# Kernel tuning notes

Measured on AMD Instinct MI355X. Metric: run time of the kernel, lower is better.

The kernel has to match this reference:

```python
import jax, jax.numpy as jnp
import numpy as np

N_NODES = 50000
N_EDGES = 600000
N_SUB = 20000
E_SUB = 120000
D = 128

def setup_inputs() -> dict:
    key = jax.random.key(0)
    ks = jax.random.split(key, 16)
    s = 1.0 / np.sqrt(D)
    inp = {
        "x": jax.random.normal(ks[0], (N_NODES, D), dtype=jnp.float32),
        "Wm": jax.random.normal(ks[1], (D, D), dtype=jnp.float32) * s,
        "bm": jnp.zeros((D,), dtype=jnp.float32),
        "Wn2s0": jax.random.normal(ks[2], (D, D), dtype=jnp.float32) * s,
        "bn2s0": jnp.zeros((D,), dtype=jnp.float32),
        "Ws2n0": jax.random.normal(ks[3], (D, D), dtype=jnp.float32) * s,
        "bs2n0": jnp.zeros((D,), dtype=jnp.float32),
        "Wn2s1": jax.random.normal(ks[4], (D, D), dtype=jnp.float32) * s,
        "bn2s1": jnp.zeros((D,), dtype=jnp.float32),
        "Ws2n1": jax.random.normal(ks[5], (D, D), dtype=jnp.float32) * s,
        "bs2n1": jnp.zeros((D,), dtype=jnp.float32),
        "neighbor_edge_index": jax.random.randint(ks[6], (2, N_EDGES), 0, N_NODES, dtype=jnp.int64),
        "sub_row0": jax.random.randint(ks[7], (E_SUB,), 0, N_NODES, dtype=jnp.int64),
        "sub_col0": jax.random.randint(ks[8], (E_SUB,), 0, N_SUB, dtype=jnp.int64),
        "sub_row1": jax.random.randint(ks[9], (E_SUB,), 0, N_NODES, dtype=jnp.int64),
        "sub_col1": jax.random.randint(ks[10], (E_SUB,), 0, N_SUB, dtype=jnp.int64),
    }
    return inp


def _level(x, row, col, Wn2s, bn2s, Ws2n, bs2n):
    # node -> substructure: gather node feats, sum-reduce into substructures
    sub_x = jax.ops.segment_sum(x[row], col, num_segments=N_SUB)  # [n_sub, D]
    sub_x = sub_x @ Wn2s + bn2s
    # substructure -> node: gather substructure feats, sum-reduce back to nodes
    msg = jax.ops.segment_sum(sub_x[col], row, num_segments=N_NODES)  # [N, D]
    msg = msg @ Ws2n + bs2n
    return x + msg


def reference(x, Wm, bm, Wn2s0, bn2s0, Ws2n0, bs2n0, Wn2s1, bn2s1, Ws2n1, bs2n1,
              neighbor_edge_index, sub_row0, sub_col0, sub_row1, sub_col1):
    src, dst = neighbor_edge_index[0], neighbor_edge_index[1]
    # message_neighbor: GIN-like sum aggregation + Linear + ReLU
    agg = jax.ops.segment_sum(x[src], dst, num_segments=N_NODES)
    x = jax.nn.relu((x + agg) @ Wm + bm)
    # substructure levels (gather -> scatter-sum -> Linear -> gather -> scatter-sum -> Linear -> residual)
    x = _level(x, sub_row0, sub_col0, Wn2s0, bn2s0, Ws2n0, bs2n0)
    x = _level(x, sub_row1, sub_col1, Wn2s1, bn2s1, Ws2n1, bs2n1)
    return x
```

## Files before the change

kernel.cpp:

```cpp
#include <hip/hip_runtime.h>

#define D 128
#define NN 50000
#define NS 20000
#define NNP 50048
#define NSP 20032
#define L_TOT (3 * NN + 2 * NS)
#define LDA 136

#define NB_BKT 188
#define CBUF_SLOTS 1296384
#define HIST_CHUNK 4096
#define HIST_BLOCKS 264

typedef short s16x8 __attribute__((ext_vector_type(8)));
typedef float f32x4 __attribute__((ext_vector_type(4)));

__device__ __forceinline__ float b2f(unsigned int u) {
    u <<= 16;
    float f; __builtin_memcpy(&f, &u, 4);
    return f;
}
__device__ __forceinline__ unsigned short f2b(float f) {
    unsigned int u; __builtin_memcpy(&u, &f, 4);
    u += 0x7fffu + ((u >> 16) & 1u);
    return (unsigned short)(u >> 16);
}
__device__ __forceinline__ void acc8(float* a, uint4 v) {
    a[0] += b2f(v.x & 0xffffu); a[1] += b2f(v.x >> 16);
    a[2] += b2f(v.y & 0xffffu); a[3] += b2f(v.y >> 16);
    a[4] += b2f(v.z & 0xffffu); a[5] += b2f(v.z >> 16);
    a[6] += b2f(v.w & 0xffffu); a[7] += b2f(v.w >> 16);
}

__device__ __forceinline__ void bkt_geom(int b, int& capOff, int& cap) {
    if (b < 98)       { capOff = b * 7168;                  cap = 7168; }
    else if (b < 118) { capOff = 702464  + (b - 98)  * 7168; cap = 7168; }
    else if (b < 143) { capOff = 845824  + (b - 118) * 6144; cap = 6144; }
    else if (b < 163) { capOff = 999424  + (b - 143) * 7168; cap = 7168; }
    else              { capOff = 1142784 + (b - 163) * 6144; cap = 6144; }
}

#define NX4 (NN * D / 4)
#define NW  (5 * 16384)
#define PREP_N (NX4 + NW)
#define PREP_BLOCKS ((PREP_N + 255) / 256)

struct PrepHistArgs {
    const float* x; unsigned short* xb;
    const float* w[5]; unsigned short* wt[5];
    const int* s0; const int* s1; const int* s2; const int* s3; const int* s4;
    const int* v0; const int* v1; const int* v2; const int* v3; const int* v4;
    unsigned int* coarse;
    int* cursor;
    int nE, eS, tot;
};
__global__ __launch_bounds__(256) void preph_k(PrepHistArgs p)
{
    __shared__ int cnt_l[NB_BKT];
    __shared__ int gb_l[NB_BKT];
    __shared__ int rk_l[NB_BKT];

    int bid = blockIdx.x;
    int tid = threadIdx.x;
    if (bid < PREP_BLOCKS) {
        int i = bid * 256 + tid;
        if (i < NX4) {
            float4 v = ((const float4*)p.x)[i];
            ushort4 o;
            o.x = f2b(v.x); o.y = f2b(v.y); o.z = f2b(v.z); o.w = f2b(v.w);
            ((ushort4*)p.xb)[i] = o;
            return;
        }
        i -= NX4;
        if (i < NW) {
            int wi = i >> 14;
            int r  = i & 16383;
            int k = r >> 7, n = r & 127;
            p.wt[wi][n * 128 + k] = f2b(p.w[wi][k * 128 + n]);
        }
        return;
    }

    int e0 = (bid - PREP_BLOCKS) * HIST_CHUNK;
    unsigned int pk[16];
    int bk[16];
    #pragma unroll
    for (int i = 0; i < 16; ++i) {
        int e = e0 + i * 256 + tid;
        bk[i] = -1;
        if (e < p.tot) {
            int seg, val, region;
            if (e < p.nE) { seg = p.s0[e]; val = p.v0[e]; region = 0; }
            else {
                int r = e - p.nE;
                if      (r <     p.eS) { seg = p.s1[r];            val = p.v1[r];            region = 1; }
                else if (r < 2 * p.eS) { seg = p.s2[r - p.eS];     val = p.v2[r - p.eS];     region = 2; }
                else if (r < 3 * p.eS) { seg = p.s3[r - 2 * p.eS]; val = p.v3[r - 2 * p.eS]; region = 3; }
                else                   { seg = p.s4[r - 3 * p.eS]; val = p.v4[r - 3 * p.eS]; region = 4; }
            }
            int shift, bktBase;
            if      (region == 0) { shift = 9;  bktBase = 0;   }
            else if (region == 1) { shift = 10; bktBase = 98;  }
            else if (region == 2) { shift = 11; bktBase = 118; }
            else if (region == 3) { shift = 10; bktBase = 143; }
            else                  { shift = 11; bktBase = 163; }
            int lb = seg & ((1 << shift) - 1);
            bk[i] = bktBase + (seg >> shift);
            pk[i] = ((unsigned int)lb << 16) | (unsigned int)(val & 0xffff);
        }
    }
    if (tid < NB_BKT) cnt_l[tid] = 0;
    __syncthreads();
    #pragma unroll
    for (int i = 0; i < 16; ++i)
        if (bk[i] >= 0) atomicAdd(&cnt_l[bk[i]], 1);
    __syncthreads();
    if (tid < NB_BKT) {
        int c = cnt_l[tid];
        gb_l[tid] = (c > 0) ? atomicAdd(&p.cursor[tid], c) : 0;
        rk_l[tid] = 0;
    }
    __syncthreads();
    #pragma unroll
    for (int i = 0; i < 16; ++i) {
        if (bk[i] >= 0) {
            int b = bk[i];
            int r = atomicAdd(&rk_l[b], 1);
            int pos = gb_l[b] + r;
            int capOff, cap;
            bkt_geom(b, capOff, cap);
            if (pos < cap) p.coarse[capOff + pos] = pk[i];
        }
    }
}

__global__ __launch_bounds__(256) void bscan_k(const int* __restrict__ cursor,
                                               int* __restrict__ bucketBase,
                                               int* __restrict__ offsets)
{
    __shared__ int lds[256];
    int tid = threadIdx.x;
    lds[tid] = (tid < NB_BKT) ? cursor[tid] : 0;
    __syncthreads();
    for (int off = 1; off < 256; off <<= 1) {
        int t = (tid >= off) ? lds[tid - off] : 0;
        __syncthreads();
        lds[tid] += t;
        __syncthreads();
    }
    if (tid < NB_BKT) bucketBase[tid] = (tid > 0) ? lds[tid - 1] : 0;
    if (tid == 0) offsets[0] = 0;
}

__global__ __launch_bounds__(256) void fine_k(
    const unsigned int* __restrict__ coarse, const int* __restrict__ cursor,
    const int* __restrict__ bucketBase, int* __restrict__ offsets,
    unsigned short* __restrict__ perm)
{
    __shared__ int hist[2048];
    __shared__ int cur[2048];
    __shared__ int part[256];

    int b = blockIdx.x;
    int tid = threadIdx.x;

    int bIn, shift, regionBins, gBinBase;
    if (b < 98)       { bIn = b;       shift = 9;  regionBins = NN; gBinBase = 0; }
    else if (b < 118) { bIn = b - 98;  shift = 10; regionBins = NS; gBinBase = NN; }
    else if (b < 143) { bIn = b - 118; shift = 11; regionBins = NN; gBinBase = NN + NS; }
    else if (b < 163) { bIn = b - 143; shift = 10; regionBins = NS; gBinBase = 2 * NN + NS; }
    else              { bIn = b - 163; shift = 11; regionBins = NN; gBinBase = 2 * NN + 2 * NS; }
    int BS = 1 << shift;
    int localBinBase = bIn << shift;
    int nb = regionBins - localBinBase; if (nb > BS) nb = BS;
    int g0 = gBinBase + localBinBase;
    int capOff, cap;
    bkt_geom(b, capOff, cap);
    const unsigned int* src = coarse + capOff;
    int cnt = cursor[b]; if (cnt > cap) cnt = cap;
    int permBase = bucketBase[b];

    for (int i = tid; i < 2048; i += 256) hist[i] = 0;
    __syncthreads();
    for (int i = tid; i < cnt; i += 256)
        atomicAdd(&hist[src[i] >> 16], 1);
    __syncthreads();

    int base8 = tid * 8;
    int loc[8]; int s = 0;
    #pragma unroll
    for (int j = 0; j < 8; ++j) { loc[j] = hist[base8 + j]; s += loc[j]; }
    part[tid] = s;
    __syncthreads();
    for (int off = 1; off < 256; off <<= 1) {
        int t = (tid >= off) ? part[tid - off] : 0;
        __syncthreads();
        part[tid] += t;
        __syncthreads();
    }
    int run = (tid > 0) ? part[tid - 1] : 0;
    #pragma unroll
    for (int j = 0; j < 8; ++j) { cur[base8 + j] = run; run += loc[j]; }
    __syncthreads();

    for (int i = tid; i < nb; i += 256)
        offsets[g0 + i + 1] = permBase + cur[i] + hist[i];
    __syncthreads();

    for (int i = tid; i < cnt; i += 256) {
        unsigned int w = src[i];
        int lb = (int)(w >> 16);
        int pos = atomicAdd(&cur[lb], 1);
        perm[permBase + pos] = (unsigned short)(w & 0xffffu);
    }
}

__global__ __launch_bounds__(256, 7) void gg_k(
    const unsigned short* __restrict__ feat, const int* __restrict__ offsets,
    const unsigned short* __restrict__ perm, const unsigned short* __restrict__ addend,
    const unsigned short* __restrict__ Wt, const float* __restrict__ bias,
    const unsigned short* __restrict__ Rb,
    float* __restrict__ outF, unsigned short* __restrict__ outB,
    int M, int relu)
{
    __shared__ unsigned short a_lds[64 * LDA];

    const int tid = threadIdx.x;
    const int r0  = blockIdx.x * 64;

    const uint4* f4 = (const uint4*)feat;
    const int lane16 = tid & 15;
    #pragma unroll
    for (int p = 0; p < 4; ++p) {
        int rloc = p * 16 + (tid >> 4);
        int s = r0 + rloc;
        float a[8] = {0.f, 0.f, 0.f, 0.f, 0.f, 0.f, 0.f, 0.f};
        if (s < M) {
            float b[8] = {0.f, 0.f, 0.f, 0.f, 0.f, 0.f, 0.f, 0.f};
            if (addend) {
                uint4 v = ((const uint4*)(addend + (size_t)s * D))[lane16];
                acc8(a, v);
            }
            int beg = offsets[s], end = offsets[s + 1];
            int j = beg;
            for (; j + 3 < end; j += 4) {
                int e0 = perm[j], e1 = perm[j + 1], e2 = perm[j + 2], e3 = perm[j + 3];
                uint4 v0 = f4[(size_t)e0 * 16 + lane16];
                uint4 v1 = f4[(size_t)e1 * 16 + lane16];
                uint4 v2 = f4[(size_t)e2 * 16 + lane16];
                uint4 v3 = f4[(size_t)e3 * 16 + lane16];
                acc8(a, v0); acc8(b, v1); acc8(a, v2); acc8(b, v3);
            }
            for (; j < end; ++j)
                acc8(a, f4[(size_t)perm[j] * 16 + lane16]);
            #pragma unroll
            for (int i = 0; i < 8; ++i) a[i] += b[i];
        }
        uint4 o;
        o.x = (unsigned int)f2b(a[0]) | ((unsigned int)f2b(a[1]) << 16);
        o.y = (unsigned int)f2b(a[2]) | ((unsigned int)f2b(a[3]) << 16);
        o.z = (unsigned int)f2b(a[4]) | ((unsigned int)f2b(a[5]) << 16);
        o.w = (unsigned int)f2b(a[6]) | ((unsigned int)f2b(a[7]) << 16);
        *((uint4*)&a_lds[rloc * LDA + lane16 * 8]) = o;
    }
    __syncthreads();

    const int lane = tid & 63;
    const int w    = tid >> 6;
    const int ln   = lane & 15;
    const int quad = lane >> 4;

    s16x8 af[4];
    const unsigned short* arow = &a_lds[(w * 16 + ln) * LDA + quad * 8];
    #pragma unroll
    for (int kc = 0; kc < 4; ++kc)
        af[kc] = *((const s16x8*)(arow + kc * 32));

    const int rbase = r0 + w * 16 + quad * 4;
    const s16x8* wt8 = (const s16x8*)Wt;

    #pragma unroll
    for (int nt = 0; nt < 8; ++nt) {
        f32x4 acc = {0.f, 0.f, 0.f, 0.f};
        const s16x8* brow = wt8 + (nt * 16 + ln) * 16 + quad;
        #pragma unroll
        for (int kc = 0; kc < 4; ++kc) {
            s16x8 bf = brow[kc * 4];
            acc = __builtin_amdgcn_mfma_f32_16x16x32_bf16(af[kc], bf, acc, 0, 0, 0);
        }
        int col = nt * 16 + ln;
        float bc = bias[col];
        #pragma unroll
        for (int r = 0; r < 4; ++r) {
            int row = rbase + r;
            if (row < M) {
                float v = acc[r] + bc;
                size_t gi = (size_t)row * D + col;
                if (Rb) v += b2f((unsigned int)Rb[gi]);
                if (relu) v = fmaxf(v, 0.f);
                if (outF) outF[gi] = v;
                if (outB) outB[gi] = f2b(v);
            }
        }
    }
}

extern "C" void kernel_launch(void* const* d_in, const int* in_sizes, int n_in,
                              void* d_out, int out_size, void* d_ws, size_t ws_size,
                              hipStream_t stream)
{
    const float* x     = (const float*)d_in[0];
    const float* Wm    = (const float*)d_in[1];
    const float* bm    = (const float*)d_in[2];
    const float* Wn2s0 = (const float*)d_in[3];
    const float* bn2s0 = (const float*)d_in[4];
    const float* Ws2n0 = (const float*)d_in[5];
    const float* bs2n0 = (const float*)d_in[6];
    const float* Wn2s1 = (const float*)d_in[7];
    const float* bn2s1 = (const float*)d_in[8];
    const float* Ws2n1 = (const float*)d_in[9];
    const float* bs2n1 = (const float*)d_in[10];
    const int* nei  = (const int*)d_in[11];
    const int* row0 = (const int*)d_in[12];
    const int* col0 = (const int*)d_in[13];
    const int* row1 = (const int*)d_in[14];
    const int* col1 = (const int*)d_in[15];

    const int N_E = in_sizes[11] / 2;
    const int E_S = in_sizes[12];
    const int TOT_E = N_E + 4 * E_S;

    const int* src = nei;
    const int* dst = nei + N_E;

    float* out = (float*)d_out;

    unsigned short* xb   = (unsigned short*)d_ws;
    unsigned short* hbf  = xb  + (size_t)NNP * D;
    unsigned short* subb = hbf + (size_t)NNP * D;
    unsigned short* wtb  = subb + (size_t)NSP * D;
    unsigned short* perm = wtb + 5 * 16384;
    int* ip = (int*)(perm + ((TOT_E + 1) & ~1));
    unsigned int* coarse = (unsigned int*)ip; ip += CBUF_SLOTS;
    int* cursor     = ip;  ip += 192;
    int* bucketBase = ip;  ip += 192;
    int* offsets    = ip;  ip += L_TOT + 1;

    unsigned short* wt0 = wtb;
    unsigned short* wt1 = wtb + 16384;
    unsigned short* wt2 = wtb + 2 * 16384;
    unsigned short* wt3 = wtb + 3 * 16384;
    unsigned short* wt4 = wtb + 4 * 16384;

    const int* offB  = offsets;
    const int* off0c = offsets + NN;
    const int* off0r = offsets + NN + NS;
    const int* off1c = offsets + 2 * NN + NS;
    const int* off1r = offsets + 2 * NN + 2 * NS;

    dim3 blk(256);
    dim3 gGemmN(NNP / 64);
    dim3 gGemmS(NSP / 64);
    dim3 gPrepH(PREP_BLOCKS + HIST_BLOCKS);

    hipMemsetAsync(cursor, 0, 192 * sizeof(int), stream);
    PrepHistArgs pa;
    pa.x = x; pa.xb = xb;
    pa.w[0] = Wm;  pa.w[1] = Wn2s0; pa.w[2] = Ws2n0; pa.w[3] = Wn2s1; pa.w[4] = Ws2n1;
    pa.wt[0] = wt0; pa.wt[1] = wt1; pa.wt[2] = wt2; pa.wt[3] = wt3; pa.wt[4] = wt4;
    pa.s0 = dst;  pa.s1 = col0; pa.s2 = row0; pa.s3 = col1; pa.s4 = row1;
    pa.v0 = src;  pa.v1 = row0; pa.v2 = col0; pa.v3 = row1; pa.v4 = col1;
    pa.coarse = coarse; pa.cursor = cursor;
    pa.nE = N_E; pa.eS = E_S; pa.tot = TOT_E;
    preph_k<<<gPrepH, blk, 0, stream>>>(pa);

    bscan_k<<<1, blk, 0, stream>>>(cursor, bucketBase, offsets);
    fine_k<<<NB_BKT, blk, 0, stream>>>(coarse, cursor, bucketBase, offsets, perm);

    gg_k<<<gGemmN, blk, 0, stream>>>(xb, offB, perm, xb, wt0, bm,
                                     nullptr, nullptr, hbf, NN, 1);

    gg_k<<<gGemmS, blk, 0, stream>>>(hbf, off0c, perm, nullptr, wt1, bn2s0,
                                     nullptr, nullptr, subb, NS, 0);
    gg_k<<<gGemmN, blk, 0, stream>>>(subb, off0r, perm, nullptr, wt2, bs2n0,
                                     hbf, nullptr, xb, NN, 0);

    gg_k<<<gGemmS, blk, 0, stream>>>(xb, off1c, perm, nullptr, wt3, bn2s1,
                                     nullptr, nullptr, subb, NS, 0);
    gg_k<<<gGemmN, blk, 0, stream>>>(subb, off1r, perm, nullptr, wt4, bs2n1,
                                     xb, out, nullptr, NN, 0);
}
```

Measured before the change: 314.7 us.

## Use 512-thread blocks in fused gather-GEMM and widen gather unroll to 8

The fused gather+GEMM kernel now runs 512 threads per 64-row tile. Each thread gathers 2 rows instead of 4, and the 8 waves split the 128 output columns into two halves of 64. The gather inner loop also gets an 8-way unrolled path so more independent loads are in flight per thread. The aim is more memory-level parallelism and latency hiding in the irregular gather. The cost is higher register pressure under launch_bounds(512,6) and fewer resident blocks per CU.

```diff
diff --git a/kernel.cpp b/kernel.cpp
--- a/kernel.cpp
+++ b/kernel.cpp
@@ -216,7 +216,7 @@
     }
 }
 
-__global__ __launch_bounds__(256, 7) void gg_k(
+__global__ __launch_bounds__(512, 6) void gg_k(
     const unsigned short* __restrict__ feat, const int* __restrict__ offsets,
     const unsigned short* __restrict__ perm, const unsigned short* __restrict__ addend,
     const unsigned short* __restrict__ Wt, const float* __restrict__ bias,
@@ -232,8 +232,8 @@
     const uint4* f4 = (const uint4*)feat;
     const int lane16 = tid & 15;
     #pragma unroll
-    for (int p = 0; p < 4; ++p) {
-        int rloc = p * 16 + (tid >> 4);
+    for (int p = 0; p < 2; ++p) {
+        int rloc = p * 32 + (tid >> 4);
         int s = r0 + rloc;
         float a[8] = {0.f, 0.f, 0.f, 0.f, 0.f, 0.f, 0.f, 0.f};
         if (s < M) {
@@ -244,6 +244,20 @@
             }
             int beg = offsets[s], end = offsets[s + 1];
             int j = beg;
+            for (; j + 7 < end; j += 8) {
+                int e0 = perm[j],     e1 = perm[j + 1], e2 = perm[j + 2], e3 = perm[j + 3];
+                int e4 = perm[j + 4], e5 = perm[j + 5], e6 = perm[j + 6], e7 = perm[j + 7];
+                uint4 v0 = f4[(size_t)e0 * 16 + lane16];
+                uint4 v1 = f4[(size_t)e1 * 16 + lane16];
+                uint4 v2 = f4[(size_t)e2 * 16 + lane16];
+                uint4 v3 = f4[(size_t)e3 * 16 + lane16];
+                uint4 v4 = f4[(size_t)e4 * 16 + lane16];
+                uint4 v5 = f4[(size_t)e5 * 16 + lane16];
+                uint4 v6 = f4[(size_t)e6 * 16 + lane16];
+                uint4 v7 = f4[(size_t)e7 * 16 + lane16];
+                acc8(a, v0); acc8(b, v1); acc8(a, v2); acc8(b, v3);
+                acc8(a, v4); acc8(b, v5); acc8(a, v6); acc8(b, v7);
+            }
             for (; j + 3 < end; j += 4) {
                 int e0 = perm[j], e1 = perm[j + 1], e2 = perm[j + 2], e3 = perm[j + 3];
                 uint4 v0 = f4[(size_t)e0 * 16 + lane16];
@@ -268,28 +282,30 @@
 
     const int lane = tid & 63;
     const int w    = tid >> 6;
+    const int wr   = w & 3;
+    const int wc   = w >> 2;
     const int ln   = lane & 15;
     const int quad = lane >> 4;
 
     s16x8 af[4];
-    const unsigned short* arow = &a_lds[(w * 16 + ln) * LDA + quad * 8];
+    const unsigned short* arow = &a_lds[(wr * 16 + ln) * LDA + quad * 8];
     #pragma unroll
     for (int kc = 0; kc < 4; ++kc)
         af[kc] = *((const s16x8*)(arow + kc * 32));
 
-    const int rbase = r0 + w * 16 + quad * 4;
+    const int rbase = r0 + wr * 16 + quad * 4;
     const s16x8* wt8 = (const s16x8*)Wt;
 
     #pragma unroll
-    for (int nt = 0; nt < 8; ++nt) {
+    for (int nt = 0; nt < 4; ++nt) {
         f32x4 acc = {0.f, 0.f, 0.f, 0.f};
-        const s16x8* brow = wt8 + (nt * 16 + ln) * 16 + quad;
+        int col = wc * 64 + nt * 16 + ln;
+        const s16x8* brow = wt8 + col * 16 + quad;
         #pragma unroll
         for (int kc = 0; kc < 4; ++kc) {
             s16x8 bf = brow[kc * 4];
             acc = __builtin_amdgcn_mfma_f32_16x16x32_bf16(af[kc], bf, acc, 0, 0, 0);
         }
-        int col = nt * 16 + ln;
         float bc = bias[col];
         #pragma unroll
         for (int r = 0; r < 4; ++r) {
@@ -360,6 +376,7 @@
     const int* off1r = offsets + 2 * NN + 2 * NS;
 
     dim3 blk(256);
+    dim3 blkG(512);
     dim3 gGemmN(NNP / 64);
     dim3 gGemmS(NSP / 64);
     dim3 gPrepH(PREP_BLOCKS + HIST_BLOCKS);
@@ -378,16 +395,16 @@
     bscan_k<<<1, blk, 0, stream>>>(cursor, bucketBase, offsets);
     fine_k<<<NB_BKT, blk, 0, stream>>>(coarse, cursor, bucketBase, offsets, perm);
 
-    gg_k<<<gGemmN, blk, 0, stream>>>(xb, offB, perm, xb, wt0, bm,
-                                     nullptr, nullptr, hbf, NN, 1);
-
-    gg_k<<<gGemmS, blk, 0, stream>>>(hbf, off0c, perm, nullptr, wt1, bn2s0,
-                                     nullptr, nullptr, subb, NS, 0);
-    gg_k<<<gGemmN, blk, 0, stream>>>(subb, off0r, perm, nullptr, wt2, bs2n0,
-                                     hbf, nullptr, xb, NN, 0);
-
-    gg_k<<<gGemmS, blk, 0, stream>>>(xb, off1c, perm, nullptr, wt3, bn2s1,
-                                     nullptr, nullptr, subb, NS, 0);
-    gg_k<<<gGemmN, blk, 0, stream>>>(subb, off1r, perm, nullptr, wt4, bs2n1,
-                                     xb, out, nullptr, NN, 0);
-}
+    gg_k<<<gGemmN, blkG, 0, stream>>>(xb, offB, perm, xb, wt0, bm,
+                                      nullptr, nullptr, hbf, NN, 1);
+
+    gg_k<<<gGemmS, blkG, 0, stream>>>(hbf, off0c, perm, nullptr, wt1, bn2s0,
+                                      nullptr, nullptr, subb, NS, 0);
+    gg_k<<<gGemmN, blkG, 0, stream>>>(subb, off0r, perm, nullptr, wt2, bs2n0,
+                                      hbf, nullptr, xb, NN, 0);
+
+    gg_k<<<gGemmS, blkG, 0, stream>>>(xb, off1c, perm, nullptr, wt3, bn2s1,
+                                      nullptr, nullptr, subb, NS, 0);
+    gg_k<<<gGemmN, blkG, 0, stream>>>(subb, off1r, perm, nullptr, wt4, bs2n1,
+                                      xb, out, nullptr, NN, 0);
+}
```

New measurement: 305.4 us. 1.03x faster.

## Fuse all stages into one cooperative persistent kernel with grid syncs

Applied to the files above, without the earlier changes.

Replaces the eight separate kernel launches (prep/histogram, bucket scan, fine sort, five gather-GEMM stages) with a single cooperative kernel that loops over virtual blocks and uses grid.sync between phases. The bucket scan is folded into each fine-sort block, and the gather loop gets an 8-way unrolled path for more loads in flight. The aim is to remove launch gaps and tail effects between the many short stages. In exchange the grid is capped at 1024 persistent blocks with at most 4 per CU under launch bounds, which may lower occupancy for the memory-bound gather stages, and grid barriers add their own cost. A multi-launch fallback is kept.

```diff
diff --git a/kernel.cpp b/kernel.cpp
--- a/kernel.cpp
+++ b/kernel.cpp
@@ -1,4 +1,7 @@
 #include <hip/hip_runtime.h>
+#include <hip/hip_cooperative_groups.h>
+
+namespace cg = cooperative_groups;
 
 #define D 128
 #define NN 50000
@@ -13,6 +16,11 @@
 #define HIST_CHUNK 4096
 #define HIST_BLOCKS 264
 
+#define NX4 (NN * D / 4)
+#define NW  (5 * 16384)
+#define PREP_BLOCKS ((NX4 + NW + 255) / 256)
+#define NV1 (PREP_BLOCKS + HIST_BLOCKS)
+
 typedef short s16x8 __attribute__((ext_vector_type(8)));
 typedef float f32x4 __attribute__((ext_vector_type(4)));
 
@@ -41,129 +49,118 @@
     else              { capOff = 1142784 + (b - 163) * 6144; cap = 6144; }
 }
 
-#define NX4 (NN * D / 4)
-#define NW  (5 * 16384)
-#define PREP_N (NX4 + NW)
-#define PREP_BLOCKS ((PREP_N + 255) / 256)
-
-struct PrepHistArgs {
+struct MegaArgs {
     const float* x; unsigned short* xb;
     const float* w[5]; unsigned short* wt[5];
-    const int* s0; const int* s1; const int* s2; const int* s3; const int* s4;
-    const int* v0; const int* v1; const int* v2; const int* v3; const int* v4;
-    unsigned int* coarse;
-    int* cursor;
+    const float* bias[5];
+    const int* s[5]; const int* v[5];
+    unsigned int* coarse; int* cursor;
+    int* offsets; unsigned short* perm;
+    unsigned short* hbf; unsigned short* subb;
+    float* out;
     int nE, eS, tot;
 };
-__global__ __launch_bounds__(256) void preph_k(PrepHistArgs p)
-{
-    __shared__ int cnt_l[NB_BKT];
-    __shared__ int gb_l[NB_BKT];
-    __shared__ int rk_l[NB_BKT];
-
-    int bid = blockIdx.x;
-    int tid = threadIdx.x;
-    if (bid < PREP_BLOCKS) {
-        int i = bid * 256 + tid;
-        if (i < NX4) {
-            float4 v = ((const float4*)p.x)[i];
-            ushort4 o;
-            o.x = f2b(v.x); o.y = f2b(v.y); o.z = f2b(v.z); o.w = f2b(v.w);
-            ((ushort4*)p.xb)[i] = o;
-            return;
-        }
-        i -= NX4;
-        if (i < NW) {
-            int wi = i >> 14;
-            int r  = i & 16383;
-            int k = r >> 7, n = r & 127;
-            p.wt[wi][n * 128 + k] = f2b(p.w[wi][k * 128 + n]);
-        }
-        return;
-    }
-
-    int e0 = (bid - PREP_BLOCKS) * HIST_CHUNK;
-    unsigned int pk[16];
-    int bk[16];
-    #pragma unroll
-    for (int i = 0; i < 16; ++i) {
-        int e = e0 + i * 256 + tid;
-        bk[i] = -1;
-        if (e < p.tot) {
-            int seg, val, region;
-            if (e < p.nE) { seg = p.s0[e]; val = p.v0[e]; region = 0; }
-            else {
-                int r = e - p.nE;
-                if      (r <     p.eS) { seg = p.s1[r];            val = p.v1[r];            region = 1; }
-                else if (r < 2 * p.eS) { seg = p.s2[r - p.eS];     val = p.v2[r - p.eS];     region = 2; }
-                else if (r < 3 * p.eS) { seg = p.s3[r - 2 * p.eS]; val = p.v3[r - 2 * p.eS]; region = 3; }
-                else                   { seg = p.s4[r - 3 * p.eS]; val = p.v4[r - 3 * p.eS]; region = 4; }
-            }
-            int shift, bktBase;
-            if      (region == 0) { shift = 9;  bktBase = 0;   }
-            else if (region == 1) { shift = 10; bktBase = 98;  }
-            else if (region == 2) { shift = 11; bktBase = 118; }
-            else if (region == 3) { shift = 10; bktBase = 143; }
-            else                  { shift = 11; bktBase = 163; }
-            int lb = seg & ((1 << shift) - 1);
-            bk[i] = bktBase + (seg >> shift);
-            pk[i] = ((unsigned int)lb << 16) | (unsigned int)(val & 0xffff);
-        }
-    }
-    if (tid < NB_BKT) cnt_l[tid] = 0;
-    __syncthreads();
-    #pragma unroll
-    for (int i = 0; i < 16; ++i)
-        if (bk[i] >= 0) atomicAdd(&cnt_l[bk[i]], 1);
-    __syncthreads();
-    if (tid < NB_BKT) {
-        int c = cnt_l[tid];
-        gb_l[tid] = (c > 0) ? atomicAdd(&p.cursor[tid], c) : 0;
-        rk_l[tid] = 0;
-    }
-    __syncthreads();
-    #pragma unroll
-    for (int i = 0; i < 16; ++i) {
-        if (bk[i] >= 0) {
-            int b = bk[i];
-            int r = atomicAdd(&rk_l[b], 1);
-            int pos = gb_l[b] + r;
-            int capOff, cap;
-            bkt_geom(b, capOff, cap);
-            if (pos < cap) p.coarse[capOff + pos] = pk[i];
-        }
-    }
-}
-
-__global__ __launch_bounds__(256) void bscan_k(const int* __restrict__ cursor,
-                                               int* __restrict__ bucketBase,
-                                               int* __restrict__ offsets)
-{
-    __shared__ int lds[256];
-    int tid = threadIdx.x;
-    lds[tid] = (tid < NB_BKT) ? cursor[tid] : 0;
-    __syncthreads();
-    for (int off = 1; off < 256; off <<= 1) {
-        int t = (tid >= off) ? lds[tid - off] : 0;
-        __syncthreads();
-        lds[tid] += t;
-        __syncthreads();
-    }
-    if (tid < NB_BKT) bucketBase[tid] = (tid > 0) ? lds[tid - 1] : 0;
-    if (tid == 0) offsets[0] = 0;
-}
-
-__global__ __launch_bounds__(256) void fine_k(
-    const unsigned int* __restrict__ coarse, const int* __restrict__ cursor,
-    const int* __restrict__ bucketBase, int* __restrict__ offsets,
-    unsigned short* __restrict__ perm)
-{
-    __shared__ int hist[2048];
-    __shared__ int cur[2048];
-    __shared__ int part[256];
-
+
+__device__ void prep_phase(char* smem, const MegaArgs& a)
+{
+    int* cnt_l = (int*)smem;
+    int* gb_l  = cnt_l + NB_BKT;
+    int* rk_l  = gb_l  + NB_BKT;
+    const int tid = threadIdx.x;
+
+    for (int vb = blockIdx.x; vb < NV1; vb += gridDim.x) {
+        if (vb < PREP_BLOCKS) {
+            int i = vb * 256 + tid;
+            if (i < NX4) {
+                float4 v = ((const float4*)a.x)[i];
+                ushort4 o;
+                o.x = f2b(v.x); o.y = f2b(v.y); o.z = f2b(v.z); o.w = f2b(v.w);
+                ((ushort4*)a.xb)[i] = o;
+            } else {
+                i -= NX4;
+                if (i < NW) {
+                    int wi = i >> 14;
+                    int r  = i & 16383;
+                    int k = r >> 7, n = r & 127;
+                    a.wt[wi][n * 128 + k] = f2b(a.w[wi][k * 128 + n]);
+                }
+            }
+            continue;
+        }
+
+        int e0 = (vb - PREP_BLOCKS) * HIST_CHUNK;
+        unsigned int pk[16];
+        int bk[16];
+        #pragma unroll
+        for (int i = 0; i < 16; ++i) {
+            int e = e0 + i * 256 + tid;
+            bk[i] = -1;
+            if (e < a.tot) {
+                int seg, val, region;
+                if (e < a.nE) { seg = a.s[0][e]; val = a.v[0][e]; region = 0; }
+                else {
+                    int r = e - a.nE;
+                    if      (r <     a.eS) { seg = a.s[1][r];            val = a.v[1][r];            region = 1; }
+                    else if (r < 2 * a.eS) { seg = a.s[2][r - a.eS];     val = a.v[2][r - a.eS];     region = 2; }
+                    else if (r < 3 * a.eS) { seg = a.s[3][r - 2 * a.eS]; val = a.v[3][r - 2 * a.eS]; region = 3; }
+                    else                   { seg = a.s[4][r - 3 * a.eS]; val = a.v[4][r - 3 * a.eS]; region = 4; }
+                }
+                int shift, bktBase;
+                if      (region == 0) { shift = 9;  bktBase = 0;   }
+                else if (region == 1) { shift = 10; bktBase = 98;  }
+                else if (region == 2) { shift = 11; bktBase = 118; }
+                else if (region == 3) { shift = 10; bktBase = 143; }
+                else                  { shift = 11; bktBase = 163; }
+                int lb = seg & ((1 << shift) - 1);
+                bk[i] = bktBase + (seg >> shift);
+                pk[i] = ((unsigned int)lb << 16) | (unsigned int)(val & 0xffff);
+            }
+        }
+        if (tid < NB_BKT) cnt_l[tid] = 0;
+        __syncthreads();
+        #pragma unroll
+        for (int i = 0; i < 16; ++i)
+            if (bk[i] >= 0) atomicAdd(&cnt_l[bk[i]], 1);
+        __syncthreads();
+        if (tid < NB_BKT) {
+            int c = cnt_l[tid];
+            gb_l[tid] = (c > 0) ? atomicAdd(&a.cursor[tid], c) : 0;
+            rk_l[tid] = 0;
+        }
+        __syncthreads();
+        #pragma unroll
+        for (int i = 0; i < 16; ++i) {
+            if (bk[i] >= 0) {
+                int b = bk[i];
+                int r = atomicAdd(&rk_l[b], 1);
+                int pos = gb_l[b] + r;
+                int capOff, cap;
+                bkt_geom(b, capOff, cap);
+                if (pos < cap) a.coarse[capOff + pos] = pk[i];
+            }
+        }
+        __syncthreads();
+    }
+}
+
+__device__ void fine_phase(char* smem, const MegaArgs& a)
+{
     int b = blockIdx.x;
     int tid = threadIdx.x;
+    int* hist = (int*)smem;
+    int* cur  = hist + 2048;
+    int* part = cur + 2048;
+
+    part[tid] = (tid < NB_BKT) ? a.cursor[tid] : 0;
+    __syncthreads();
+    for (int off = 1; off < 256; off <<= 1) {
+        int t = (tid >= off) ? part[tid - off] : 0;
+        __syncthreads();
+        part[tid] += t;
+        __syncthreads();
+    }
+    int permBase = (b > 0) ? part[b - 1] : 0;
+    __syncthreads();
 
     int bIn, shift, regionBins, gBinBase;
     if (b < 98)       { bIn = b;       shift = 9;  regionBins = NN; gBinBase = 0; }
@@ -177,9 +174,8 @@
     int g0 = gBinBase + localBinBase;
     int capOff, cap;
     bkt_geom(b, capOff, cap);
-    const unsigned int* src = coarse + capOff;
-    int cnt = cursor[b]; if (cnt > cap) cnt = cap;
-    int permBase = bucketBase[b];
+    const unsigned int* src = a.coarse + capOff;
+    int cnt = a.cursor[b]; if (cnt > cap) cnt = cap;
 
     for (int i = tid; i < 2048; i += 256) hist[i] = 0;
     __syncthreads();
@@ -205,106 +201,187 @@
     __syncthreads();
 
     for (int i = tid; i < nb; i += 256)
-        offsets[g0 + i + 1] = permBase + cur[i] + hist[i];
+        a.offsets[g0 + i + 1] = permBase + cur[i] + hist[i];
     __syncthreads();
 
     for (int i = tid; i < cnt; i += 256) {
         unsigned int w = src[i];
         int lb = (int)(w >> 16);
         int pos = atomicAdd(&cur[lb], 1);
-        perm[permBase + pos] = (unsigned short)(w & 0xffffu);
-    }
-}
-
-__global__ __launch_bounds__(256, 7) void gg_k(
-    const unsigned short* __restrict__ feat, const int* __restrict__ offsets,
-    const unsigned short* __restrict__ perm, const unsigned short* __restrict__ addend,
+        a.perm[permBase + pos] = (unsigned short)(w & 0xffffu);
+    }
+    if (b == 0 && tid == 0) a.offsets[0] = 0;
+}
+
+__device__ void gg_phase(
+    char* smem, const unsigned short* __restrict__ feat,
+    const int* __restrict__ offsets, const unsigned short* __restrict__ perm,
+    const unsigned short* __restrict__ addend,
     const unsigned short* __restrict__ Wt, const float* __restrict__ bias,
     const unsigned short* __restrict__ Rb,
     float* __restrict__ outF, unsigned short* __restrict__ outB,
-    int M, int relu)
-{
-    __shared__ unsigned short a_lds[64 * LDA];
-
+    int M, int relu, int ntiles)
+{
+    unsigned short* a_lds = (unsigned short*)smem;
     const int tid = threadIdx.x;
-    const int r0  = blockIdx.x * 64;
-
     const uint4* f4 = (const uint4*)feat;
     const int lane16 = tid & 15;
-    #pragma unroll
-    for (int p = 0; p < 4; ++p) {
-        int rloc = p * 16 + (tid >> 4);
-        int s = r0 + rloc;
-        float a[8] = {0.f, 0.f, 0.f, 0.f, 0.f, 0.f, 0.f, 0.f};
-        if (s < M) {
-            float b[8] = {0.f, 0.f, 0.f, 0.f, 0.f, 0.f, 0.f, 0.f};
-            if (addend) {
-                uint4 v = ((const uint4*)(addend + (size_t)s * D))[lane16];
-                acc8(a, v);
-            }
-            int beg = offsets[s], end = offsets[s + 1];
-            int j = beg;
-            for (; j + 3 < end; j += 4) {
-                int e0 = perm[j], e1 = perm[j + 1], e2 = perm[j + 2], e3 = perm[j + 3];
-                uint4 v0 = f4[(size_t)e0 * 16 + lane16];
-                uint4 v1 = f4[(size_t)e1 * 16 + lane16];
-                uint4 v2 = f4[(size_t)e2 * 16 + lane16];
-                uint4 v3 = f4[(size_t)e3 * 16 + lane16];
-                acc8(a, v0); acc8(b, v1); acc8(a, v2); acc8(b, v3);
-            }
-            for (; j < end; ++j)
-                acc8(a, f4[(size_t)perm[j] * 16 + lane16]);
+
+    for (int t = blockIdx.x; t < ntiles; t += gridDim.x) {
+        const int r0 = t * 64;
+
+        #pragma unroll
+        for (int p = 0; p < 4; ++p) {
+            int rloc = p * 16 + (tid >> 4);
+            int s = r0 + rloc;
+            float acc_a[8] = {0.f, 0.f, 0.f, 0.f, 0.f, 0.f, 0.f, 0.f};
+            if (s < M) {
+                float acc_b[8] = {0.f, 0.f, 0.f, 0.f, 0.f, 0.f, 0.f, 0.f};
+                if (addend) {
+                    uint4 v = ((const uint4*)(addend + (size_t)s * D))[lane16];
+                    acc8(acc_a, v);
+                }
+                int beg = offsets[s], end = offsets[s + 1];
+                int j = beg;
+                for (; j + 7 < end; j += 8) {
+                    int e0 = perm[j],     e1 = perm[j + 1], e2 = perm[j + 2], e3 = perm[j + 3];
+                    int e4 = perm[j + 4], e5 = perm[j + 5], e6 = perm[j + 6], e7 = perm[j + 7];
+                    uint4 v0 = f4[(size_t)e0 * 16 + lane16];
+                    uint4 v1 = f4[(size_t)e1 * 16 + lane16];
+                    uint4 v2 = f4[(size_t)e2 * 16 + lane16];
+                    uint4 v3 = f4[(size_t)e3 * 16 + lane16];
+                    uint4 v4 = f4[(size_t)e4 * 16 + lane16];
+                    uint4 v5 = f4[(size_t)e5 * 16 + lane16];
+                    uint4 v6 = f4[(size_t)e6 * 16 + lane16];
+                    uint4 v7 = f4[(size_t)e7 * 16 + lane16];
+                    acc8(acc_a, v0); acc8(acc_b, v1); acc8(acc_a, v2); acc8(acc_b, v3);
+                    acc8(acc_a, v4); acc8(acc_b, v5); acc8(acc_a, v6); acc8(acc_b, v7);
+                }
+                for (; j + 3 < end; j += 4) {
+                    int e0 = perm[j], e1 = perm[j + 1], e2 = perm[j + 2], e3 = perm[j + 3];
+                    uint4 v0 = f4[(size_t)e0 * 16 + lane16];
+                    uint4 v1 = f4[(size_t)e1 * 16 + lane16];
+                    uint4 v2 = f4[(size_t)e2 * 16 + lane16];
+                    uint4 v3 = f4[(size_t)e3 * 16 + lane16];
+                    acc8(acc_a, v0); acc8(acc_b, v1); acc8(acc_a, v2); acc8(acc_b, v3);
+                }
+                for (; j < end; ++j)
+                    acc8(acc_a, f4[(size_t)perm[j] * 16 + lane16]);
+                #pragma unroll
+                for (int i = 0; i < 8; ++i) acc_a[i] += acc_b[i];
+            }
+            uint4 o;
+            o.x = (unsigned int)f2b(acc_a[0]) | ((unsigned int)f2b(acc_a[1]) << 16);
+            o.y = (unsigned int)f2b(acc_a[2]) | ((unsigned int)f2b(acc_a[3]) << 16);
+            o.z = (unsigned int)f2b(acc_a[4]) | ((unsigned int)f2b(acc_a[5]) << 16);
+            o.w = (unsigned int)f2b(acc_a[6]) | ((unsigned int)f2b(acc_a[7]) << 16);
+            *((uint4*)&a_lds[rloc * LDA + lane16 * 8]) = o;
+        }
+        __syncthreads();
+
+        const int lane = tid & 63;
+        const int w    = tid >> 6;
+        const int ln   = lane & 15;
+        const int quad = lane >> 4;
+
+        s16x8 af[4];
+        const unsigned short* arow = &a_lds[(w * 16 + ln) * LDA + quad * 8];
+        #pragma unroll
+        for (int kc = 0; kc < 4; ++kc)
+            af[kc] = *((const s16x8*)(arow + kc * 32));
+
+        const int rbase = r0 + w * 16 + quad * 4;
+        const s16x8* wt8 = (const s16x8*)Wt;
+
+        #pragma unroll
+        for (int nt = 0; nt < 8; ++nt) {
+            f32x4 acc = {0.f, 0.f, 0.f, 0.f};
+            const s16x8* brow = wt8 + (nt * 16 + ln) * 16 + quad;
             #pragma unroll
-            for (int i = 0; i < 8; ++i) a[i] += b[i];
-        }
-        uint4 o;
-        o.x = (unsigned int)f2b(a[0]) | ((unsigned int)f2b(a[1]) << 16);
-        o.y = (unsigned int)f2b(a[2]) | ((unsigned int)f2b(a[3]) << 16);
-        o.z = (unsigned int)f2b(a[4]) | ((unsigned int)f2b(a[5]) << 16);
-        o.w = (unsigned int)f2b(a[6]) | ((unsigned int)f2b(a[7]) << 16);
-        *((uint4*)&a_lds[rloc * LDA + lane16 * 8]) = o;
-    }
-    __syncthreads();
-
-    const int lane = tid & 63;
-    const int w    = tid >> 6;
-    const int ln   = lane & 15;
-    const int quad = lane >> 4;
-
-    s16x8 af[4];
-    const unsigned short* arow = &a_lds[(w * 16 + ln) * LDA + quad * 8];
-    #pragma unroll
-    for (int kc = 0; kc < 4; ++kc)
-        af[kc] = *((const s16x8*)(arow + kc * 32));
-
-    const int rbase = r0 + w * 16 + quad * 4;
-    const s16x8* wt8 = (const s16x8*)Wt;
-
-    #pragma unroll
-    for (int nt = 0; nt < 8; ++nt) {
-        f32x4 acc = {0.f, 0.f, 0.f, 0.f};
-        const s16x8* brow = wt8 + (nt * 16 + ln) * 16 + quad;
-        #pragma unroll
-        for (int kc = 0; kc < 4; ++kc) {
-            s16x8 bf = brow[kc * 4];
-            acc = __builtin_amdgcn_mfma_f32_16x16x32_bf16(af[kc], bf, acc, 0, 0, 0);
-        }
-        int col = nt * 16 + ln;
-        float bc = bias[col];
-        #pragma unroll
-        for (int r = 0; r < 4; ++r) {
-            int row = rbase + r;
-            if (row < M) {
-                float v = acc[r] + bc;
-                size_t gi = (size_t)row * D + col;
-                if (Rb) v += b2f((unsigned int)Rb[gi]);
-                if (relu) v = fmaxf(v, 0.f);
-                if (outF) outF[gi] = v;
-                if (outB) outB[gi] = f2b(v);
-            }
-        }
-    }
-}
+            for (int kc = 0; kc < 4; ++kc) {
+                s16x8 bf = brow[kc * 4];
+                acc = __builtin_amdgcn_mfma_f32_16x16x32_bf16(af[kc], bf, acc, 0, 0, 0);
+            }
+            int col = nt * 16 + ln;
+            float bc = bias[col];
+            #pragma unroll
+            for (int r = 0; r < 4; ++r) {
+                int row = rbase + r;
+                if (row < M) {
+                    float v = acc[r] + bc;
+                    size_t gi = (size_t)row * D + col;
+                    if (Rb) v += b2f((unsigned int)Rb[gi]);
+                    if (relu) v = fmaxf(v, 0.f);
+                    if (outF) outF[gi] = v;
+                    if (outB) outB[gi] = f2b(v);
+                }
+            }
+        }
+        __syncthreads();
+    }
+}
+
+__device__ void dispatch_gg(char* smem, const MegaArgs& a, int which)
+{
+    switch (which) {
+    case 0:
+        gg_phase(smem, a.xb, a.offsets, a.perm, a.xb, a.wt[0], a.bias[0],
+                 nullptr, nullptr, a.hbf, NN, 1, NNP / 64);
+        break;
+    case 1:
+        gg_phase(smem, a.hbf, a.offsets + NN, a.perm, nullptr, a.wt[1], a.bias[1],
+                 nullptr, nullptr, a.subb, NS, 0, NSP / 64);
+        break;
+    case 2:
+        gg_phase(smem, a.subb, a.offsets + NN + NS, a.perm, nullptr, a.wt[2], a.bias[2],
+                 a.hbf, nullptr, a.xb, NN, 0, NNP / 64);
+        break;
+    case 3:
+        gg_phase(smem, a.xb, a.offsets + 2 * NN + NS, a.perm, nullptr, a.wt[3], a.bias[3],
+                 nullptr, nullptr, a.subb, NS, 0, NSP / 64);
+        break;
+    default:
+        gg_phase(smem, a.subb, a.offsets + 2 * NN + 2 * NS, a.perm, nullptr, a.wt[4], a.bias[4],
+                 a.xb, a.out, nullptr, NN, 0, NNP / 64);
+        break;
+    }
+}
+
+__global__ __launch_bounds__(256, 4) void mega_k(MegaArgs a)
+{
+    __shared__ __align__(16) char smem[17408];
+    cg::grid_group grid = cg::this_grid();
+
+    prep_phase(smem, a);
+    grid.sync();
+
+    if (blockIdx.x < NB_BKT) fine_phase(smem, a);
+    grid.sync();
+
+    #pragma unroll 1
+    for (int s = 0; s < 5; ++s) {
+        dispatch_gg(smem, a, s);
+        if (s < 4) grid.sync();
+    }
+}
+
+__global__ __launch_bounds__(256) void fb_prep_k(MegaArgs a)
+{
+    __shared__ __align__(16) char smem[17408];
+    prep_phase(smem, a);
+}
+__global__ __launch_bounds__(256) void fb_sort_k(MegaArgs a)
+{
+    __shared__ __align__(16) char smem[17408];
+    fine_phase(smem, a);
+}
+__global__ __launch_bounds__(256) void fb_gg_k(MegaArgs a, int which)
+{
+    __shared__ __align__(16) char smem[17408];
+    dispatch_gg(smem, a, which);
+}
+
+static int g_coopBlocks = -2;
 
 extern "C" void kernel_launch(void* const* d_in, const int* in_sizes, int n_in,
                               void* d_out, int out_size, void* d_ws, size_t ws_size,
@@ -344,50 +421,53 @@
     int* ip = (int*)(perm + ((TOT_E + 1) & ~1));
     unsigned int* coarse = (unsigned int*)ip; ip += CBUF_SLOTS;
     int* cursor     = ip;  ip += 192;
-    int* bucketBase = ip;  ip += 192;
     int* offsets    = ip;  ip += L_TOT + 1;
 
-    unsigned short* wt0 = wtb;
-    unsigned short* wt1 = wtb + 16384;
-    unsigned short* wt2 = wtb + 2 * 16384;
-    unsigned short* wt3 = wtb + 3 * 16384;
-    unsigned short* wt4 = wtb + 4 * 16384;
-
-    const int* offB  = offsets;
-    const int* off0c = offsets + NN;
-    const int* off0r = offsets + NN + NS;
-    const int* off1c = offsets + 2 * NN + NS;
-    const int* off1r = offsets + 2 * NN + 2 * NS;
+    MegaArgs ma;
+    ma.x = x; ma.xb = xb;
+    ma.w[0] = Wm;  ma.w[1] = Wn2s0; ma.w[2] = Ws2n0; ma.w[3] = Wn2s1; ma.w[4] = Ws2n1;
+    ma.wt[0] = wtb;             ma.wt[1] = wtb + 16384;     ma.wt[2] = wtb + 2 * 16384;
+    ma.wt[3] = wtb + 3 * 16384; ma.wt[4] = wtb + 4 * 16384;
+    ma.bias[0] = bm; ma.bias[1] = bn2s0; ma.bias[2] = bs2n0; ma.bias[3] = bn2s1; ma.bias[4] = bs2n1;
+    ma.s[0] = dst;  ma.s[1] = col0; ma.s[2] = row0; ma.s[3] = col1; ma.s[4] = row1;
+    ma.v[0] = src;  ma.v[1] = row0; ma.v[2] = col0; ma.v[3] = row1; ma.v[4] = col1;
+    ma.coarse = coarse; ma.cursor = cursor;
+    ma.offsets = offsets; ma.perm = perm;
+    ma.hbf = hbf; ma.subb = subb; ma.out = out;
+    ma.nE = N_E; ma.eS = E_S; ma.tot = TOT_E;
+
+    if (g_coopBlocks == -2) {
+        int coop = 0, perCU = 0, nCU = 0;
+        if (hipDeviceGetAttribute(&coop, hipDeviceAttributeCooperativeLaunch, 0) != hipSuccess) coop = 0;
+        if (hipDeviceGetAttribute(&nCU, hipDeviceAttributeMultiprocessorCount, 0) != hipSuccess) nCU = 0;
+        if (coop && nCU > 0 &&
+            hipOccupancyMaxActiveBlocksPerMultiprocessor(&perCU, mega_k, 256, 0) == hipSuccess &&
+            perCU > 0) {
+            long g = (long)perCU * nCU;
+            if (g > 1024) g = 1024;
+            g_coopBlocks = (g >= 256) ? (int)g : 0;
+        } else {
+            g_coopBlocks = 0;
+        }
+    }
+
+    hipMemsetAsync(cursor, 0, 192 * sizeof(int), stream);
+
+    if (g_coopBlocks > 0) {
+        void* kargs[] = { (void*)&ma };
+        hipError_t e = hipLaunchCooperativeKernel((const void*)mega_k,
+                                                  dim3(g_coopBlocks), dim3(256),
+                                                  kargs, 0, stream);
+        if (e == hipSuccess) return;
+        g_coopBlocks = 0;
+    }
 
     dim3 blk(256);
-    dim3 gGemmN(NNP / 64);
-    dim3 gGemmS(NSP / 64);
-    dim3 gPrepH(PREP_BLOCKS + HIST_BLOCKS);
-
-    hipMemsetAsync(cursor, 0, 192 * sizeof(int), stream);
-    PrepHistArgs pa;
-    pa.x = x; pa.xb = xb;
-    pa.w[0] = Wm;  pa.w[1] = Wn2s0; pa.w[2] = Ws2n0; pa.w[3] = Wn2s1; pa.w[4] = Ws2n1;
-    pa.wt[0] = wt0; pa.wt[1] = wt1; pa.wt[2] = wt2; pa.wt[3] = wt3; pa.wt[4] = wt4;
-    pa.s0 = dst;  pa.s1 = col0; pa.s2 = row0; pa.s3 = col1; pa.s4 = row1;
-    pa.v0 = src;  pa.v1 = row0; pa.v2 = col0; pa.v3 = row1; pa.v4 = col1;
-    pa.coarse = coarse; pa.cursor = cursor;
-    pa.nE = N_E; pa.eS = E_S; pa.tot = TOT_E;
-    preph_k<<<gPrepH, blk, 0, stream>>>(pa);
-
-    bscan_k<<<1, blk, 0, stream>>>(cursor, bucketBase, offsets);
-    fine_k<<<NB_BKT, blk, 0, stream>>>(coarse, cursor, bucketBase, offsets, perm);
-
-    gg_k<<<gGemmN, blk, 0, stream>>>(xb, offB, perm, xb, wt0, bm,
-                                     nullptr, nullptr, hbf, NN, 1);
-
-    gg_k<<<gGemmS, blk, 0, stream>>>(hbf, off0c, perm, nullptr, wt1, bn2s0,
-                                     nullptr, nullptr, subb, NS, 0);
-    gg_k<<<gGemmN, blk, 0, stream>>>(subb, off0r, perm, nullptr, wt2, bs2n0,
-                                     hbf, nullptr, xb, NN, 0);
-
-    gg_k<<<gGemmS, blk, 0, stream>>>(xb, off1c, perm, nullptr, wt3, bn2s1,
-                                     nullptr, nullptr, subb, NS, 0);
-    gg_k<<<gGemmN, blk, 0, stream>>>(subb, off1r, perm, nullptr, wt4, bs2n1,
-                                     xb, out, nullptr, NN, 0);
-}
+    fb_prep_k<<<NV1, blk, 0, stream>>>(ma);
+    fb_sort_k<<<NB_BKT, blk, 0, stream>>>(ma);
+    fb_gg_k<<<NNP / 64, blk, 0, stream>>>(ma, 0);
+    fb_gg_k<<<NSP / 64, blk, 0, stream>>>(ma, 1);
+    fb_gg_k<<<NNP / 64, blk, 0, stream>>>(ma, 2);
+    fb_gg_k<<<NSP / 64, blk, 0, stream>>>(ma, 3);
+    fb_gg_k<<<NNP / 64, blk, 0, stream>>>(ma, 4);
+}
```

Result: slower. 509.6 us (+61.9%).
